# Kernel tuning notes

Measured on AMD Instinct MI355X. Metric: run time of the kernel, lower is better.

Reference implementation:

```python
import jax, jax.numpy as jnp
import numpy as np

HIDDEN = 4096
N_HEADS = 32
HEAD_DIM = HIDDEN // N_HEADS  # 128
ROPE_BASE = 10000.0


def _rotate_half(x):
    h = x.shape[-1] // 2
    return jnp.concatenate((-x[..., h:], x[..., :h]), axis=-1)


def _rope_sin_cos(position_ids):
    # position_ids: [B, S] int -> sin, cos: [B, 1, S, head_dim]
    inv_freq = 1.0 / (ROPE_BASE ** (jnp.arange(0, HEAD_DIM, 2, dtype=jnp.float32) / HEAD_DIM))
    freqs = position_ids.astype(jnp.float32)[..., None] * inv_freq  # [B,S,hd/2]
    emb = jnp.concatenate((freqs, freqs), axis=-1)  # [B,S,hd]
    return jnp.sin(emb)[:, None, :, :], jnp.cos(emb)[:, None, :, :]


def setup_inputs() -> dict:
    key = jax.random.key(0)
    k1, k2, k3 = jax.random.split(key, 3)
    B, S = 2, 2048
    hidden_states = jax.random.normal(k1, (B, S, HIDDEN), dtype=jnp.float32)
    w_qkv = jax.random.normal(k2, (HIDDEN, 3 * HIDDEN), dtype=jnp.float32) * 0.02
    wo = jax.random.normal(k3, (HIDDEN, HIDDEN), dtype=jnp.float32) * 0.02
    position_ids = jnp.broadcast_to(jnp.arange(S, dtype=jnp.int32)[None, :], (B, S))
    return {"hidden_states": hidden_states, "w_qkv": w_qkv, "wo": wo,
            "position_ids": position_ids}


def reference(hidden_states, w_qkv, wo, position_ids):
    B, S, H = hidden_states.shape
    qkv = hidden_states @ w_qkv  # [B,S,3H]
    q, k, v = jnp.split(qkv, 3, axis=-1)
    # [B,S,nH,hd] -> [B,nH,S,hd]
    q = q.reshape(B, S, N_HEADS, HEAD_DIM).transpose(0, 2, 1, 3)
    k = k.reshape(B, S, N_HEADS, HEAD_DIM).transpose(0, 2, 1, 3)
    v = v.reshape(B, S, N_HEADS, HEAD_DIM).transpose(0, 2, 1, 3)
    sin, cos = _rope_sin_cos(position_ids)  # [B,1,S,hd]
    q = q * cos + _rotate_half(q) * sin
    k = k * cos + _rotate_half(k) * sin
    scale = 1.0 / np.sqrt(HEAD_DIM)
    scores = jnp.einsum('bhqd,bhkd->bhqk', q, k) * scale
    causal = jnp.tril(jnp.ones((S, S), dtype=bool))
    scores = jnp.where(causal[None, None, :, :], scores, jnp.finfo(scores.dtype).min)
    attn = jax.nn.softmax(scores, axis=-1)
    out = jnp.einsum('bhqk,bhkd->bhqd', attn, v)  # [B,nH,S,hd]
    out = out.transpose(0, 2, 1, 3).reshape(B, S, H)
    return out @ wo
```

## Files before the change

kernel.cpp:

```cpp
#include <hip/hip_runtime.h>

typedef unsigned int u32;
typedef unsigned short u16;
typedef short short8 __attribute__((ext_vector_type(8)));
typedef float f32x4 __attribute__((ext_vector_type(4)));
typedef unsigned short us4 __attribute__((ext_vector_type(4)));

#define S_LEN 2048
#define BATCH 2
#define HID 4096
#define NH 32
#define HD 128
#define TRIH 12288

#define GCAST(p) ((const __attribute__((address_space(1))) u32*)(p))
#define LCAST(p) ((__attribute__((address_space(3))) u32*)(p))

static __device__ __forceinline__ u16 f2bf(float f) {
  union { float f; u32 u; } x; x.f = f;
  u32 u = x.u;
  u32 r = u + 0x7FFFu + ((u >> 16) & 1u);
  return (u16)(r >> 16);
}
static __device__ __forceinline__ float bf2f(u16 h) {
  union { u32 u; float f; } x; x.u = ((u32)h) << 16;
  return x.f;
}

__global__ __launch_bounds__(256) void cvt_f32_bf16(const float* __restrict__ in,
                                                    u16* __restrict__ out, int n4) {
  int i = blockIdx.x * 256 + threadIdx.x;
  if (i >= n4) return;
  float4 v = ((const float4*)in)[i];
  us4 o;
  o.x = f2bf(v.x); o.y = f2bf(v.y); o.z = f2bf(v.z); o.w = f2bf(v.w);
  ((us4*)out)[i] = o;
}

__global__ __launch_bounds__(256) void tr_cvt(const float* __restrict__ in,
                                              u16* __restrict__ out, int R, int C) {
  __shared__ float tile[32][33];
  int c0 = blockIdx.x * 32, r0 = blockIdx.y * 32;
  int tx = threadIdx.x, ty = threadIdx.y;
  for (int i = ty; i < 32; i += 8)
    tile[i][tx] = in[(size_t)(r0 + i) * C + c0 + tx];
  __syncthreads();
  for (int i = ty; i < 32; i += 8)
    out[(size_t)(c0 + i) * R + r0 + tx] = f2bf(tile[tx][i]);
}


template<int MQ, int NQ>
static __device__ __forceinline__ void mfma_quad(f32x4 (&acc)[8][4], short8 (&af)[4][2],
                                                 short8 (&bfr)[4][2]) {
#pragma unroll
  for (int ml = 0; ml < 4; ++ml)
#pragma unroll
    for (int nl = 0; nl < 2; ++nl) {
      acc[MQ*4+ml][NQ*2+nl] = __builtin_amdgcn_mfma_f32_16x16x32_bf16(
          af[ml][0], bfr[NQ*2+nl][0], acc[MQ*4+ml][NQ*2+nl], 0, 0, 0);
      acc[MQ*4+ml][NQ*2+nl] = __builtin_amdgcn_mfma_f32_16x16x32_bf16(
          af[ml][1], bfr[NQ*2+nl][1], acc[MQ*4+ml][NQ*2+nl], 0, 0, 0);
    }
}

template<int MQ>
static __device__ __forceinline__ void read_a(short8 (&af)[4][2], const u16* abase, int lane) {
#pragma unroll
  for (int ml = 0; ml < 4; ++ml) {
    int r = MQ*64 + ml*16 + (lane & 15);
#pragma unroll
    for (int kh = 0; kh < 2; ++kh) {
      int j = kh*4 + (lane >> 4);
      af[ml][kh] = *(const short8*)(abase + r*64 + ((j ^ (r & 7)) << 3));
    }
  }
}
template<int NQ>
static __device__ __forceinline__ void read_b(short8 (&bfr)[4][2], const u16* bbase,
                                              int rbase, int lane) {
#pragma unroll
  for (int nl = 0; nl < 2; ++nl) {
    int r = rbase + (NQ*2+nl)*16 + (lane & 15);
#pragma unroll
    for (int kh = 0; kh < 2; ++kh) {
      int j = kh*4 + (lane >> 4);
      bfr[NQ*2+nl][kh] = *(const short8*)(bbase + r*64 + ((j ^ (r & 7)) << 3));
    }
  }
}

#define PHASE_CLOSE() \
  __builtin_amdgcn_s_barrier(); \
  __builtin_amdgcn_sched_barrier(0);

#define SEAM_CLOSE(NSTR) \
  asm volatile("s_waitcnt vmcnt(" NSTR ")" ::: "memory"); \
  __builtin_amdgcn_s_barrier(); \
  __builtin_amdgcn_sched_barrier(0);

template<int OUTF32>
__global__ __launch_bounds__(512, 1) void gemm256(const u16* __restrict__ A,
                                                  const u16* __restrict__ Bt,
                                                  void* __restrict__ Cout,
                                                  int M, int N, int K, int nbm) {
  __shared__ __attribute__((aligned(16))) u16 lds[65536];
  const int tid = threadIdx.x, wave = tid >> 6, lane = tid & 63;
  const int wr = wave >> 2, wc = wave & 3;
  const int nwg = gridDim.x, wg = blockIdx.x, cpx = nwg >> 3;
  const int swz = (wg & 7) * cpx + (wg >> 3);
  const size_t tileM = (size_t)(swz % nbm) * 256;
  const size_t tileN = (size_t)(swz / nbm) * 256;
  const int nIter = K >> 7;

  const int r_ = tid >> 3;
  const int gc_ = (tid & 7) ^ (r_ & 7);

  const u16* Ag = A + tileM * K;
  const u16* Bg = Bt + tileN * K;

  f32x4 acc[8][4] = {};
  short8 af[4][2], bfr[4][2];

  auto stageA = [&](int kt, int buf, int half) {
    const u16* g0 = Ag + (size_t)(half*128 + r_) * K + kt*64 + (gc_ << 3);
    u16* l = lds + buf*16384 + half*8192 + wave*512;
    __builtin_amdgcn_global_load_lds(GCAST(g0), LCAST(l), 16, 0, 0);
    __builtin_amdgcn_global_load_lds(GCAST(g0 + (size_t)64*K), LCAST(l + 4096), 16, 0, 0);
  };
  auto stageB = [&](int kt, int buf, int half) {
    const u16* g0 = Bg + (size_t)(half*128 + r_) * K + kt*64 + (gc_ << 3);
    u16* l = lds + 32768 + buf*16384 + half*8192 + wave*512;
    __builtin_amdgcn_global_load_lds(GCAST(g0), LCAST(l), 16, 0, 0);
    __builtin_amdgcn_global_load_lds(GCAST(g0 + (size_t)64*K), LCAST(l + 4096), 16, 0, 0);
  };

  const u16* a0 = lds + wr*8192;
  const u16* a1 = lds + 16384 + wr*8192;
  const u16* b0 = lds + 32768 + (wc >> 1)*8192;
  const u16* b1 = lds + 32768 + 16384 + (wc >> 1)*8192;
  const int brb = (wc & 1) * 64;

  stageA(0, 0, 0); stageA(0, 0, 1);
  stageB(0, 0, 0); stageB(0, 0, 1);
  stageB(1, 1, 0); stageB(1, 1, 1);
  SEAM_CLOSE("4")

  for (int i = 0; i < nIter; ++i) {
    const int t1 = 2*i + 1, t2 = 2*i + 2, t3 = 2*i + 3;
    const bool more = (i + 1 < nIter);

    read_a<0>(af, a0, lane);
    read_b<0>(bfr, b0, brb, lane);
    read_b<1>(bfr, b0, brb, lane);
    stageA(t1, 1, 0); stageA(t1, 1, 1);
    __builtin_amdgcn_s_setprio(1);
    mfma_quad<0, 0>(acc, af, bfr);
    mfma_quad<0, 1>(acc, af, bfr);
    __builtin_amdgcn_s_setprio(0);
    PHASE_CLOSE()

    read_a<1>(af, a0, lane);
    if (more) { stageB(t2, 0, 0); stageB(t2, 0, 1); }
    __builtin_amdgcn_s_setprio(1);
    mfma_quad<1, 0>(acc, af, bfr);
    mfma_quad<1, 1>(acc, af, bfr);
    __builtin_amdgcn_s_setprio(0);
    if (more) { SEAM_CLOSE("4") } else { SEAM_CLOSE("0") }

    read_a<0>(af, a1, lane);
    read_b<0>(bfr, b1, brb, lane);
    read_b<1>(bfr, b1, brb, lane);
    if (more) { stageA(t2, 0, 0); stageA(t2, 0, 1); }
    __builtin_amdgcn_s_setprio(1);
    mfma_quad<0, 0>(acc, af, bfr);
    mfma_quad<0, 1>(acc, af, bfr);
    __builtin_amdgcn_s_setprio(0);
    PHASE_CLOSE()

    read_a<1>(af, a1, lane);
    if (more) { stageB(t3, 1, 0); stageB(t3, 1, 1); }
    __builtin_amdgcn_s_setprio(1);
    mfma_quad<1, 0>(acc, af, bfr);
    mfma_quad<1, 1>(acc, af, bfr);
    __builtin_amdgcn_s_setprio(0);
    if (more) { SEAM_CLOSE("4") } else { PHASE_CLOSE() }
  }

  const int r0o = (lane >> 4) << 2, c0o = lane & 15;
#pragma unroll
  for (int m = 0; m < 8; ++m)
#pragma unroll
    for (int n = 0; n < 4; ++n)
#pragma unroll
      for (int rr = 0; rr < 4; ++rr) {
        size_t grow = tileM + wr*128 + m*16 + r0o + rr;
        size_t gcol = tileN + wc*64 + n*16 + c0o;
        if (OUTF32) ((float*)Cout)[grow * N + gcol] = acc[m][n][rr];
        else        ((u16*)Cout)[grow * N + gcol] = f2bf(acc[m][n][rr]);
      }
}

__global__ __launch_bounds__(256) void rope_kernel(u16* __restrict__ qkv,
                                                   const int* __restrict__ pid) {
  int idx = blockIdx.x * 256 + threadIdx.x;
  int row = idx >> 9;
  int rem = idx & 511;
  int which = rem >> 8;
  int h = (rem >> 3) & 31;
  int j0 = (rem & 7) << 3;
  u16* p = qkv + (size_t)row * TRIH + which * HID + h * HD + j0;
  short8 lo = *(short8*)p;
  short8 hi = *(short8*)(p + 64);
  float pos = (float)pid[row];
  short8 olo, ohi;
#pragma unroll
  for (int i = 0; i < 8; ++i) {
    float x0 = bf2f((u16)lo[i]), x1 = bf2f((u16)hi[i]);
    float th = pos * expf(-(float)(j0 + i) * 0.14391156831212787f);
    float sn, cs;
    sincosf(th, &sn, &cs);
    olo[i] = (short)f2bf(x0 * cs - x1 * sn);
    ohi[i] = (short)f2bf(x1 * cs + x0 * sn);
  }
  *(short8*)p = olo;
  *(short8*)(p + 64) = ohi;
}

__global__ __launch_bounds__(512, 2) void attn_kernel(const u16* __restrict__ qkv,
                                                      u16* __restrict__ O) {
  const int bid = blockIdx.x;
  const int qt = 15 - (bid >> 6);
  const int bh = bid & 63;
  const int b = bh >> 5, h = bh & 31;
  const int tid = threadIdx.x, wave = tid >> 6, lane = tid & 63;
  __shared__ u16 Ks[2][64 * 128];
  __shared__ u16 VsT[2][128 * 64];
  __shared__ u16 Ps[8][16 * 64];
  const u16* base = qkv + (size_t)b * S_LEN * TRIH + h * HD;

  const int rbase = (lane >> 4) << 2;
  const int cbase = lane & 15;
  const int q_lo = qt * 128;
  const int wrow0 = q_lo + wave * 16;

  short8 qf[4];
  {
    const u16* qrow = base + (size_t)(wrow0 + cbase) * TRIH;
#pragma unroll
    for (int f = 0; f < 4; ++f)
      qf[f] = *(const short8*)(qrow + ((f * 4 + (lane >> 4)) << 3));
  }

  const int tmax_w = 2 * qt + (wave >= 4 ? 1 : 0);
  const int tmax_b = 2 * qt + 1;

  float mrun[4], lrun[4];
  f32x4 accO[8] = {};
#pragma unroll
  for (int r = 0; r < 4; ++r) { mrun[r] = -1e30f; lrun[r] = 0.f; }

  short8 kreg[2], vreg[2];
  auto load_tile = [&](int t) {
    int kv = t << 6;
#pragma unroll
    for (int it = 0; it < 2; ++it) {
      int c = tid + it * 512;
      int row = c >> 4, ch = c & 15;
      const u16* src = base + (size_t)(kv + row) * TRIH + (ch << 3);
      kreg[it] = *(const short8*)(src + HID);
      vreg[it] = *(const short8*)(src + 2 * HID);
    }
  };
  auto write_tile = [&](int buf) {
#pragma unroll
    for (int it = 0; it < 2; ++it) {
      int c = tid + it * 512;
      int row = c >> 4, ch = c & 15;
      *(short8*)(Ks[buf] + row * 128 + ((ch ^ (row & 7)) << 3)) = kreg[it];
#pragma unroll
      for (int i = 0; i < 8; ++i) {
        int d = (ch << 3) + i;
        VsT[buf][d * 64 + (((row >> 3) ^ (ch & 7)) << 3) + (row & 7)] = (u16)vreg[it][i];
      }
    }
  };

  load_tile(0);
  write_tile(0);
  load_tile(1);

  for (int t = 0; t <= tmax_b; ++t) {
    const int cur = t & 1;
    __syncthreads();
    if (t < tmax_b) write_tile(cur ^ 1);
    if (t + 2 <= tmax_b) load_tile(t + 2);

    if (t > tmax_w) continue;

    f32x4 s[4] = {};
#pragma unroll
    for (int n = 0; n < 4; ++n) {
      int krow = n * 16 + cbase;
#pragma unroll
      for (int f = 0; f < 4; ++f) {
        int ch = f * 4 + (lane >> 4);
        short8 kf = *(const short8*)(Ks[cur] + krow * 128 + ((ch ^ (krow & 7)) << 3));
        s[n] = __builtin_amdgcn_mfma_f32_16x16x32_bf16(qf[f], kf, s[n], 0, 0, 0);
      }
    }
    const float scale = 0.08838834764831845f;
    const int kv0 = t << 6;
    if (t == tmax_w) {
#pragma unroll
      for (int n = 0; n < 4; ++n)
#pragma unroll
        for (int r = 0; r < 4; ++r) {
          int kvcol = kv0 + n * 16 + cbase;
          int qrow = wrow0 + rbase + r;
          s[n][r] = (kvcol <= qrow) ? s[n][r] * scale : -1e30f;
        }
    } else {
#pragma unroll
      for (int n = 0; n < 4; ++n) s[n] *= scale;
    }

    float tmax[4];
#pragma unroll
    for (int r = 0; r < 4; ++r) {
      float tm = fmaxf(fmaxf(s[0][r], s[1][r]), fmaxf(s[2][r], s[3][r]));
      tm = fmaxf(tm, __shfl_xor(tm, 1));
      tm = fmaxf(tm, __shfl_xor(tm, 2));
      tm = fmaxf(tm, __shfl_xor(tm, 4));
      tm = fmaxf(tm, __shfl_xor(tm, 8));
      tmax[r] = tm;
    }
    bool need = false;
#pragma unroll
    for (int r = 0; r < 4; ++r) need |= (tmax[r] > mrun[r] + 8.0f);
    if (__any(need)) {
#pragma unroll
      for (int r = 0; r < 4; ++r) {
        float mnew = fmaxf(mrun[r], tmax[r]);
        float corr = __expf(mrun[r] - mnew);
        float rs = 0.f;
#pragma unroll
        for (int n = 0; n < 4; ++n) { float pv = __expf(s[n][r] - mnew); s[n][r] = pv; rs += pv; }
        rs += __shfl_xor(rs, 1); rs += __shfl_xor(rs, 2);
        rs += __shfl_xor(rs, 4); rs += __shfl_xor(rs, 8);
        lrun[r] = lrun[r] * corr + rs;
        mrun[r] = mnew;
#pragma unroll
        for (int nd = 0; nd < 8; ++nd) accO[nd][r] *= corr;
      }
    } else {
#pragma unroll
      for (int r = 0; r < 4; ++r) {
        float rs = 0.f;
#pragma unroll
        for (int n = 0; n < 4; ++n) { float pv = __expf(s[n][r] - mrun[r]); s[n][r] = pv; rs += pv; }
        rs += __shfl_xor(rs, 1); rs += __shfl_xor(rs, 2);
        rs += __shfl_xor(rs, 4); rs += __shfl_xor(rs, 8);
        lrun[r] += rs;
      }
    }

    u16* Pw = (u16*)Ps[wave];
#pragma unroll
    for (int n = 0; n < 4; ++n)
#pragma unroll
      for (int r = 0; r < 4; ++r) {
        int rl = rbase + r;
        int col = n * 16 + cbase;
        Pw[rl * 64 + (((col >> 3) ^ (rl & 7)) << 3) + (col & 7)] = f2bf(s[n][r]);
      }

    short8 pa[2];
    {
      int prow = lane & 15;
#pragma unroll
      for (int f2 = 0; f2 < 2; ++f2) {
        int ch = f2 * 4 + (lane >> 4);
        pa[f2] = *(const short8*)(Pw + prow * 64 + ((ch ^ (prow & 7)) << 3));
      }
    }
#pragma unroll
    for (int nd = 0; nd < 8; ++nd) {
      int drow = nd * 16 + cbase;
#pragma unroll
      for (int f2 = 0; f2 < 2; ++f2) {
        int ch = f2 * 4 + (lane >> 4);
        short8 vb = *(const short8*)(VsT[cur] + drow * 64 + ((ch ^ ((drow >> 3) & 7)) << 3));
        accO[nd] = __builtin_amdgcn_mfma_f32_16x16x32_bf16(pa[f2], vb, accO[nd], 0, 0, 0);
      }
    }
  }

#pragma unroll
  for (int nd = 0; nd < 8; ++nd)
#pragma unroll
    for (int r = 0; r < 4; ++r) {
      int qrow = wrow0 + rbase + r;
      int col = h * HD + nd * 16 + cbase;
      O[(size_t)(b * S_LEN + qrow) * HID + col] = f2bf(accO[nd][r] / lrun[r]);
    }
}

extern "C" void kernel_launch(void* const* d_in, const int* in_sizes, int n_in,
                              void* d_out, int out_size, void* d_ws, size_t ws_size,
                              hipStream_t stream) {
  const float* hidden = (const float*)d_in[0];
  const float* w_qkv  = (const float*)d_in[1];
  const float* wo     = (const float*)d_in[2];
  const int*   pid    = (const int*)d_in[3];

  const size_t MB = 1024ull * 1024ull;
  u16* hb    = (u16*)d_ws;
  u16* wqkvT = (u16*)((char*)d_ws + 32 * MB);
  u16* woT   = (u16*)((char*)d_ws + 128 * MB);
  u16* qkvb  = (u16*)((char*)d_ws + 160 * MB);
  u16* Obuf  = hb;

  cvt_f32_bf16<<<16384, 256, 0, stream>>>(hidden, hb, (BATCH * S_LEN * HID) / 4);
  dim3 tb(32, 8);
  tr_cvt<<<dim3(TRIH / 32, HID / 32), tb, 0, stream>>>(w_qkv, wqkvT, HID, TRIH);
  tr_cvt<<<dim3(HID / 32, HID / 32), tb, 0, stream>>>(wo, woT, HID, HID);

  gemm256<0><<<768, 512, 0, stream>>>(hb, wqkvT, qkvb, BATCH * S_LEN, TRIH, HID, 16);

  rope_kernel<<<(BATCH * S_LEN * 2 * NH * 8) / 256, 256, 0, stream>>>(qkvb, pid);

  attn_kernel<<<1024, 512, 0, stream>>>(qkvb, Obuf);

  gemm256<1><<<256, 512, 0, stream>>>(Obuf, woT, d_out, BATCH * S_LEN, HID, HID, 16);
}
```

Baseline: 815.6 us.

## Vectorize weight transpose-convert and simplify GEMM pipeline to full-drain barriers

The weight transpose-convert kernel now uses 64x64 tiles with float4 global loads and 4-wide bf16 stores, so fewer and wider memory transactions move the weight bytes. The GEMM main loop drops the staggered A/B prefetch schedule, the partial vmcnt waits and the setprio hints. It now stages A and B for the next tile together and drains every load with vmcnt(0) at each half-iteration. That removes two barriers per iteration, but gives up the deeper prefetch overlap, so global load latency may be exposed more.

```diff
diff --git a/kernel.cpp b/kernel.cpp
--- a/kernel.cpp
+++ b/kernel.cpp
@@ -39,14 +39,30 @@
 
 __global__ __launch_bounds__(256) void tr_cvt(const float* __restrict__ in,
                                               u16* __restrict__ out, int R, int C) {
-  __shared__ float tile[32][33];
-  int c0 = blockIdx.x * 32, r0 = blockIdx.y * 32;
-  int tx = threadIdx.x, ty = threadIdx.y;
-  for (int i = ty; i < 32; i += 8)
-    tile[i][tx] = in[(size_t)(r0 + i) * C + c0 + tx];
+  __shared__ float tile[64][65];
+  int c0 = blockIdx.x * 64, r0 = blockIdx.y * 64;
+  int tx = threadIdx.x;
+  int rr = tx >> 4;
+  int cc = (tx & 15) << 2;
+#pragma unroll
+  for (int it = 0; it < 4; ++it) {
+    float4 v = *(const float4*)&in[(size_t)(r0 + rr + it * 16) * C + c0 + cc];
+    tile[rr + it * 16][cc + 0] = v.x;
+    tile[rr + it * 16][cc + 1] = v.y;
+    tile[rr + it * 16][cc + 2] = v.z;
+    tile[rr + it * 16][cc + 3] = v.w;
+  }
   __syncthreads();
-  for (int i = ty; i < 32; i += 8)
-    out[(size_t)(c0 + i) * R + r0 + tx] = f2bf(tile[tx][i]);
+#pragma unroll
+  for (int it = 0; it < 4; ++it) {
+    int crow = rr + it * 16;
+    us4 o;
+    o.x = f2bf(tile[cc + 0][crow]);
+    o.y = f2bf(tile[cc + 1][crow]);
+    o.z = f2bf(tile[cc + 2][crow]);
+    o.w = f2bf(tile[cc + 3][crow]);
+    *(us4*)&out[(size_t)(c0 + crow) * R + r0 + cc] = o;
+  }
 }
 
 
@@ -90,12 +106,8 @@
   }
 }
 
-#define PHASE_CLOSE() \
-  __builtin_amdgcn_s_barrier(); \
-  __builtin_amdgcn_sched_barrier(0);
-
-#define SEAM_CLOSE(NSTR) \
-  asm volatile("s_waitcnt vmcnt(" NSTR ")" ::: "memory"); \
+#define SEAM_CLOSE0() \
+  asm volatile("s_waitcnt vmcnt(0)" ::: "memory"); \
   __builtin_amdgcn_s_barrier(); \
   __builtin_amdgcn_sched_barrier(0);
 
@@ -143,48 +155,34 @@
 
   stageA(0, 0, 0); stageA(0, 0, 1);
   stageB(0, 0, 0); stageB(0, 0, 1);
-  stageB(1, 1, 0); stageB(1, 1, 1);
-  SEAM_CLOSE("4")
+  SEAM_CLOSE0()
 
   for (int i = 0; i < nIter; ++i) {
-    const int t1 = 2*i + 1, t2 = 2*i + 2, t3 = 2*i + 3;
+    const int t1 = 2*i + 1, t2 = 2*i + 2;
     const bool more = (i + 1 < nIter);
 
     read_a<0>(af, a0, lane);
     read_b<0>(bfr, b0, brb, lane);
     read_b<1>(bfr, b0, brb, lane);
     stageA(t1, 1, 0); stageA(t1, 1, 1);
-    __builtin_amdgcn_s_setprio(1);
+    stageB(t1, 1, 0); stageB(t1, 1, 1);
     mfma_quad<0, 0>(acc, af, bfr);
     mfma_quad<0, 1>(acc, af, bfr);
-    __builtin_amdgcn_s_setprio(0);
-    PHASE_CLOSE()
-
     read_a<1>(af, a0, lane);
-    if (more) { stageB(t2, 0, 0); stageB(t2, 0, 1); }
-    __builtin_amdgcn_s_setprio(1);
     mfma_quad<1, 0>(acc, af, bfr);
     mfma_quad<1, 1>(acc, af, bfr);
-    __builtin_amdgcn_s_setprio(0);
-    if (more) { SEAM_CLOSE("4") } else { SEAM_CLOSE("0") }
+    SEAM_CLOSE0()
 
     read_a<0>(af, a1, lane);
     read_b<0>(bfr, b1, brb, lane);
     read_b<1>(bfr, b1, brb, lane);
-    if (more) { stageA(t2, 0, 0); stageA(t2, 0, 1); }
-    __builtin_amdgcn_s_setprio(1);
+    if (more) { stageA(t2, 0, 0); stageA(t2, 0, 1); stageB(t2, 0, 0); stageB(t2, 0, 1); }
     mfma_quad<0, 0>(acc, af, bfr);
     mfma_quad<0, 1>(acc, af, bfr);
-    __builtin_amdgcn_s_setprio(0);
-    PHASE_CLOSE()
-
     read_a<1>(af, a1, lane);
-    if (more) { stageB(t3, 1, 0); stageB(t3, 1, 1); }
-    __builtin_amdgcn_s_setprio(1);
     mfma_quad<1, 0>(acc, af, bfr);
     mfma_quad<1, 1>(acc, af, bfr);
-    __builtin_amdgcn_s_setprio(0);
-    if (more) { SEAM_CLOSE("4") } else { PHASE_CLOSE() }
+    if (more) { SEAM_CLOSE0() }
   }
 
   const int r0o = (lane >> 4) << 2, c0o = lane & 15;
@@ -422,9 +420,8 @@
   u16* Obuf  = hb;
 
   cvt_f32_bf16<<<16384, 256, 0, stream>>>(hidden, hb, (BATCH * S_LEN * HID) / 4);
-  dim3 tb(32, 8);
-  tr_cvt<<<dim3(TRIH / 32, HID / 32), tb, 0, stream>>>(w_qkv, wqkvT, HID, TRIH);
-  tr_cvt<<<dim3(HID / 32, HID / 32), tb, 0, stream>>>(wo, woT, HID, HID);
+  tr_cvt<<<dim3(TRIH / 64, HID / 64), 256, 0, stream>>>(w_qkv, wqkvT, HID, TRIH);
+  tr_cvt<<<dim3(HID / 64, HID / 64), 256, 0, stream>>>(wo, woT, HID, HID);
 
   gemm256<0><<<768, 512, 0, stream>>>(hb, wqkvT, qkvb, BATCH * S_LEN, TRIH, HID, 16);
 
```

Result: no change. 823.7 us (+1.0%).
